# Performance work log

Hardware: AMD Instinct MI355X
Metric: run time of the kernel (lower is better)

## Reference

```python
import jax, jax.numpy as jnp
import numpy as np

USER_COUNT = 100000
ITEM_COUNT = 50000
N_NODES = USER_COUNT + ITEM_COUNT
NNZ = 4800000
EMB = 64
BATCH = 4096


def setup_inputs() -> dict:
    key = jax.random.key(0)
    k1, k2, k3, k4, k5, k6, k7 = jax.random.split(key, 7)
    return {
        "user_emb": jax.random.normal(k1, (USER_COUNT, EMB), dtype=jnp.float32),
        "item_emb": jax.random.normal(k2, (ITEM_COUNT, EMB), dtype=jnp.float32),
        "adj_vals": jax.random.uniform(k3, (NNZ,), dtype=jnp.float32),
        "adj_row": jax.random.randint(k4, (NNZ,), 0, N_NODES, dtype=jnp.int64),
        "adj_col": jax.random.randint(k5, (NNZ,), 0, N_NODES, dtype=jnp.int64),
        "users": jax.random.randint(k6, (BATCH,), 0, USER_COUNT, dtype=jnp.int64),
        "items": jax.random.randint(k7, (BATCH,), 0, ITEM_COUNT, dtype=jnp.int64),
        "n_layers": 3,
    }


def _spmm(adj_row, adj_col, adj_vals, x):
    # sparse (N,N) @ dense (N,D): gather source rows, scale by edge values, scatter-add to dest
    msgs = adj_vals[:, None] * x[adj_col]  # [nnz, D]
    return jax.ops.segment_sum(msgs, adj_row, num_segments=N_NODES)


def reference(user_emb, item_emb, adj_vals, adj_row, adj_col, users, items, n_layers):
    ego = jnp.concatenate([user_emb, item_emb], axis=0)  # [N, D]
    for _ in range(n_layers):
        ego = _spmm(adj_row, adj_col, adj_vals, ego)
    user_all = ego[:USER_COUNT]
    item_all = ego[USER_COUNT:]
    return (user_all[users], item_all[items])
```

## Files before the change

### kernel.cpp

```cpp
#include <hip/hip_runtime.h>
#include <hip/hip_bf16.h>

#define USER_COUNT 100000
#define ITEM_COUNT 50000
#define N_NODES    150000
#define EMB        64
#define BATCH      4096

#define NFINE      586
#define FSHIFT     8
#define STRIDE     8960
#define TILE_E     6400
#define NBSTRIDE   768

__device__ inline unsigned short f2bf_raw(float f) {
    __hip_bfloat16 h = __float2bfloat16(f);
    unsigned short u; __builtin_memcpy(&u, &h, 2); return u;
}

__global__ __launch_bounds__(512) void count_kernel(
        const int* __restrict__ rows, int* __restrict__ counts, int nnz) {
    __shared__ int cnt[NFINE];
    const int b = blockIdx.x, t = threadIdx.x;
    for (int f = t; f < NFINE; f += 512) cnt[f] = 0;
    __syncthreads();
    const int s = b * TILE_E, e = min(s + TILE_E, nnz);
    for (int i = s + t; i < e; i += 512)
        atomicAdd(&cnt[rows[i] >> FSHIFT], 1);
    __syncthreads();
    for (int f = t; f < NFINE; f += 512)
        counts[f * NBSTRIDE + b] = cnt[f];
}

__global__ __launch_bounds__(1024) void scan_offs(
        const int* __restrict__ counts, int* __restrict__ offs,
        int* __restrict__ tot, int nblk) {
    __shared__ int s[1024];
    const int f = blockIdx.x, t = threadIdx.x;
    const int c = (t < nblk) ? counts[f * NBSTRIDE + t] : 0;
    s[t] = c;
    __syncthreads();
    for (int o = 1; o < 1024; o <<= 1) {
        int v = (t >= o) ? s[t - o] : 0;
        __syncthreads();
        s[t] += v;
        __syncthreads();
    }
    if (t < nblk) offs[f * NBSTRIDE + t] = s[t] - c;
    if (t == 1023) tot[f] = s[1023];
}

__global__ __launch_bounds__(512) void partition_kernel(
        const float* __restrict__ vals,
        const int* __restrict__ rows,
        const int* __restrict__ cols,
        const int* __restrict__ offs,
        uint2* __restrict__ fine, int nnz) {
    __shared__ uint2 buf[TILE_E];
    __shared__ int   cnt[NFINE];
    __shared__ int   sloff[NFINE + 1];
    __shared__ int   gb[NFINE];
    __shared__ int   sscan[512];
    const int b = blockIdx.x, t = threadIdx.x;
    const int sbeg = b * TILE_E, send = min(sbeg + TILE_E, nnz);
    const int n = send - sbeg;

    for (int f = t; f < NFINE; f += 512) {
        cnt[f] = 0;
        gb[f] = f * STRIDE + offs[f * NBSTRIDE + b];
    }
    __syncthreads();
    for (int i = sbeg + t; i < send; i += 512)
        atomicAdd(&cnt[rows[i] >> FSHIFT], 1);
    __syncthreads();
    int c0 = (2 * t < NFINE) ? cnt[2 * t] : 0;
    int c1 = (2 * t + 1 < NFINE) ? cnt[2 * t + 1] : 0;
    sscan[t] = c0 + c1;
    __syncthreads();
    for (int o = 1; o < 512; o <<= 1) {
        int v = (t >= o) ? sscan[t - o] : 0;
        __syncthreads();
        sscan[t] += v;
        __syncthreads();
    }
    int base = (t == 0) ? 0 : sscan[t - 1];
    if (2 * t < NFINE) sloff[2 * t] = base;
    if (2 * t + 1 < NFINE) sloff[2 * t + 1] = base + c0;
    if (t == 511) sloff[NFINE] = sscan[511];
    __syncthreads();
    for (int f = t; f < NFINE; f += 512) cnt[f] = sloff[f];
    __syncthreads();
    for (int i = sbeg + t; i < send; i += 512) {
        int r = rows[i];
        int f = r >> FSHIFT;
        int pos = atomicAdd(&cnt[f], 1);
        buf[pos] = make_uint2(__float_as_uint(vals[i]),
                              (unsigned)cols[i] | ((unsigned)(r & 255) << 18));
    }
    __syncthreads();
    for (int idx = t; idx < n; idx += 512) {
        int lo = 0, hi = NFINE;
        while (hi - lo > 1) {
            int mid = (lo + hi) >> 1;
            if (sloff[mid] <= idx) lo = mid; else hi = mid;
        }
        fine[gb[lo] + (idx - sloff[lo])] = buf[idx];
    }
}

__global__ __launch_bounds__(256) void bucket_sort_kernel(
        const uint2* __restrict__ fine,
        const int* __restrict__ tot,
        float2* __restrict__ perm,
        uint2* __restrict__ rp) {
    __shared__ int hist[256];
    __shared__ int off[256];
    __shared__ int cur[256];
    const int f    = blockIdx.x;
    const int tid  = threadIdx.x;
    const int n    = min(tot[f], STRIDE);
    const int base = f * STRIDE;
    const uint2* src = fine + base;

    hist[tid] = 0;
    __syncthreads();
    for (int k = tid; k < n; k += 256)
        atomicAdd(&hist[(src[k].y >> 18) & 255], 1);
    __syncthreads();
    if (tid == 0) {
        int acc = 0;
        for (int j = 0; j < 256; ++j) { off[j] = acc; acc += hist[j]; }
    }
    __syncthreads();
    cur[tid] = off[tid];
    int row = (f << FSHIFT) + tid;
    if (row < N_NODES)
        rp[row] = make_uint2(base + off[tid], base + off[tid] + hist[tid]);
    __syncthreads();
    for (int k = tid; k < n; k += 256) {
        uint2 e = src[k];
        int lrow = (e.y >> 18) & 255;
        int pos = base + atomicAdd(&cur[lrow], 1);
        perm[pos] = make_float2(__uint_as_float(e.x),
                                __int_as_float((int)(e.y & 0x3FFFFu)));
    }
}

__global__ void to_bf16(const float4* __restrict__ ue,
                        const float4* __restrict__ ie,
                        uint2* __restrict__ xh) {
    int i = blockIdx.x * blockDim.x + threadIdx.x;
    const int n4 = (N_NODES * EMB) / 4;
    const int u4 = (USER_COUNT * EMB) / 4;
    if (i >= n4) return;
    float4 fv = (i < u4) ? ue[i] : ie[i - u4];
    uint2 o;
    o.x = (unsigned int)f2bf_raw(fv.x) | ((unsigned int)f2bf_raw(fv.y) << 16);
    o.y = (unsigned int)f2bf_raw(fv.z) | ((unsigned int)f2bf_raw(fv.w) << 16);
    xh[i] = o;
}

#define ACC8(U, W)                                      \
    a0 += (W) * __uint_as_float((U).x << 16);           \
    a1 += (W) * __uint_as_float((U).x & 0xffff0000u);   \
    a2 += (W) * __uint_as_float((U).y << 16);           \
    a3 += (W) * __uint_as_float((U).y & 0xffff0000u);   \
    a4 += (W) * __uint_as_float((U).z << 16);           \
    a5 += (W) * __uint_as_float((U).z & 0xffff0000u);   \
    a6 += (W) * __uint_as_float((U).w << 16);           \
    a7 += (W) * __uint_as_float((U).w & 0xffff0000u);

__global__ void spmm_bf16(const uint2* __restrict__ rp,
                          const float2* __restrict__ perm,
                          const unsigned short* __restrict__ xh,
                          unsigned short* __restrict__ yh) {
    int wid  = (blockIdx.x * blockDim.x + threadIdx.x) >> 6;
    int lane = threadIdx.x & 63;
    int g    = lane >> 3;
    int s    = lane & 7;
    int r    = (wid << 3) + g;
    if (r >= N_NODES) return;

    uint2 be = rp[r];
    int beg = (int)be.x, end = (int)be.y;

    const uint4* xv = (const uint4*)xh;
    float a0 = 0.f, a1 = 0.f, a2 = 0.f, a3 = 0.f;
    float a4 = 0.f, a5 = 0.f, a6 = 0.f, a7 = 0.f;

    int j = beg;
    for (; j + 7 < end; j += 8) {
        float2 e0 = perm[j];
        float2 e1 = perm[j + 1];
        float2 e2 = perm[j + 2];
        float2 e3 = perm[j + 3];
        float2 e4 = perm[j + 4];
        float2 e5 = perm[j + 5];
        float2 e6 = perm[j + 6];
        float2 e7 = perm[j + 7];
        uint4 u0 = xv[(((long long)__float_as_int(e0.y)) << 3) + s];
        uint4 u1 = xv[(((long long)__float_as_int(e1.y)) << 3) + s];
        uint4 u2 = xv[(((long long)__float_as_int(e2.y)) << 3) + s];
        uint4 u3 = xv[(((long long)__float_as_int(e3.y)) << 3) + s];
        uint4 u4 = xv[(((long long)__float_as_int(e4.y)) << 3) + s];
        uint4 u5 = xv[(((long long)__float_as_int(e5.y)) << 3) + s];
        uint4 u6 = xv[(((long long)__float_as_int(e6.y)) << 3) + s];
        uint4 u7 = xv[(((long long)__float_as_int(e7.y)) << 3) + s];
        ACC8(u0, e0.x) ACC8(u1, e1.x) ACC8(u2, e2.x) ACC8(u3, e3.x)
        ACC8(u4, e4.x) ACC8(u5, e5.x) ACC8(u6, e6.x) ACC8(u7, e7.x)
    }
    for (; j < end; ++j) {
        float2 e = perm[j];
        uint4 u = xv[(((long long)__float_as_int(e.y)) << 3) + s];
        ACC8(u, e.x)
    }

    uint4 o;
    o.x = (unsigned)f2bf_raw(a0) | ((unsigned)f2bf_raw(a1) << 16);
    o.y = (unsigned)f2bf_raw(a2) | ((unsigned)f2bf_raw(a3) << 16);
    o.z = (unsigned)f2bf_raw(a4) | ((unsigned)f2bf_raw(a5) << 16);
    o.w = (unsigned)f2bf_raw(a6) | ((unsigned)f2bf_raw(a7) << 16);
    ((uint4*)yh)[(((long long)r) << 3) + s] = o;
}

__global__ void spmm_batch_kernel(const uint2* __restrict__ rp,
                                  const float2* __restrict__ perm,
                                  const unsigned short* __restrict__ xh,
                                  const int* __restrict__ users,
                                  const int* __restrict__ items,
                                  float4* __restrict__ out) {
    int wid  = (blockIdx.x * blockDim.x + threadIdx.x) >> 6;
    int lane = threadIdx.x & 63;
    int g    = lane >> 3;
    int s    = lane & 7;
    int b    = (wid << 3) + g;
    if (b >= 2 * BATCH) return;
    int node = (b < BATCH) ? users[b] : (USER_COUNT + items[b - BATCH]);

    uint2 be = rp[node];
    int beg = (int)be.x, end = (int)be.y;

    const uint4* xv = (const uint4*)xh;
    float a0 = 0.f, a1 = 0.f, a2 = 0.f, a3 = 0.f;
    float a4 = 0.f, a5 = 0.f, a6 = 0.f, a7 = 0.f;

    int j = beg;
    for (; j + 3 < end; j += 4) {
        float2 e0 = perm[j];
        float2 e1 = perm[j + 1];
        float2 e2 = perm[j + 2];
        float2 e3 = perm[j + 3];
        uint4 u0 = xv[(((long long)__float_as_int(e0.y)) << 3) + s];
        uint4 u1 = xv[(((long long)__float_as_int(e1.y)) << 3) + s];
        uint4 u2 = xv[(((long long)__float_as_int(e2.y)) << 3) + s];
        uint4 u3 = xv[(((long long)__float_as_int(e3.y)) << 3) + s];
        ACC8(u0, e0.x) ACC8(u1, e1.x) ACC8(u2, e2.x) ACC8(u3, e3.x)
    }
    for (; j < end; ++j) {
        float2 e = perm[j];
        uint4 u = xv[(((long long)__float_as_int(e.y)) << 3) + s];
        ACC8(u, e.x)
    }

    out[(size_t)b * 16 + 2 * s]     = make_float4(a0, a1, a2, a3);
    out[(size_t)b * 16 + 2 * s + 1] = make_float4(a4, a5, a6, a7);
}

extern "C" void kernel_launch(void* const* d_in, const int* in_sizes, int n_in,
                              void* d_out, int out_size, void* d_ws, size_t ws_size,
                              hipStream_t stream) {
    const float* user_emb = (const float*)d_in[0];
    const float* item_emb = (const float*)d_in[1];
    const float* adj_vals = (const float*)d_in[2];
    const int*   adj_row  = (const int*)d_in[3];
    const int*   adj_col  = (const int*)d_in[4];
    const int*   users    = (const int*)d_in[5];
    const int*   items    = (const int*)d_in[6];

    const int nnz  = in_sizes[2];
    const int nblk = (nnz + TILE_E - 1) / TILE_E;

    const size_t region = (size_t)NFINE * STRIDE + 1024;

    char* p = (char*)d_ws;
    uint2* fine = (uint2*)p;
    unsigned short* xh_a = (unsigned short*)p;
    unsigned short* xh_b = xh_a + (size_t)N_NODES * EMB;
    p += region * sizeof(uint2);
    float2* perm = (float2*)p;
    p += region * sizeof(float2);
    uint2* rp = (uint2*)p;
    p += (size_t)(N_NODES + 16) * sizeof(uint2);
    int* counts = (int*)p;  p += (size_t)NFINE * NBSTRIDE * sizeof(int);
    int* offs   = (int*)p;  p += (size_t)NFINE * NBSTRIDE * sizeof(int);
    int* tot    = (int*)p;

    count_kernel<<<nblk, 512, 0, stream>>>(adj_row, counts, nnz);
    scan_offs<<<NFINE, 1024, 0, stream>>>(counts, offs, tot, nblk);
    partition_kernel<<<nblk, 512, 0, stream>>>(adj_vals, adj_row, adj_col,
                                               offs, fine, nnz);
    bucket_sort_kernel<<<NFINE, 256, 0, stream>>>(fine, tot, perm, rp);

    const int n4 = (N_NODES * EMB) / 4;
    to_bf16<<<(n4 + 255) / 256, 256, 0, stream>>>((const float4*)user_emb,
                                                  (const float4*)item_emb,
                                                  (uint2*)xh_a);

    const int spmm_blocks = (N_NODES / 8 + 3) / 4;
    spmm_bf16<<<spmm_blocks, 256, 0, stream>>>(rp, perm, xh_a, xh_b);
    spmm_bf16<<<spmm_blocks, 256, 0, stream>>>(rp, perm, xh_b, xh_a);
    spmm_batch_kernel<<<(2 * BATCH / 8) / 4, 256, 0, stream>>>(
        rp, perm, xh_a, users, items, (float4*)d_out);
}
```

Baseline: 440.6 us.

## Replace two-level bucket sort with global-atomic counting sort for CSR build

```diff
diff --git a/kernel.cpp b/kernel.cpp
--- a/kernel.cpp
+++ b/kernel.cpp
@@ -7,142 +7,114 @@
 #define EMB        64
 #define BATCH      4096
 
-#define NFINE      586
-#define FSHIFT     8
-#define STRIDE     8960
-#define TILE_E     6400
-#define NBSTRIDE   768
+#define SCAN_BLOCKS 147
 
 __device__ inline unsigned short f2bf_raw(float f) {
     __hip_bfloat16 h = __float2bfloat16(f);
     unsigned short u; __builtin_memcpy(&u, &h, 2); return u;
 }
 
-__global__ __launch_bounds__(512) void count_kernel(
-        const int* __restrict__ rows, int* __restrict__ counts, int nnz) {
-    __shared__ int cnt[NFINE];
-    const int b = blockIdx.x, t = threadIdx.x;
-    for (int f = t; f < NFINE; f += 512) cnt[f] = 0;
+__global__ __launch_bounds__(256) void zero_kernel(int* __restrict__ p, int n) {
+    int i = blockIdx.x * blockDim.x + threadIdx.x;
+    if (i < n) p[i] = 0;
+}
+
+__global__ __launch_bounds__(256) void degree_kernel(
+        const int* __restrict__ rows, int* __restrict__ deg, int nnz) {
+    const int tid = blockIdx.x * blockDim.x + threadIdx.x;
+    const int nth = gridDim.x * blockDim.x;
+    const int n4  = nnz >> 2;
+    const int4* r4 = (const int4*)rows;
+    for (int i = tid; i < n4; i += nth) {
+        int4 r = r4[i];
+        atomicAdd(&deg[r.x], 1);
+        atomicAdd(&deg[r.y], 1);
+        atomicAdd(&deg[r.z], 1);
+        atomicAdd(&deg[r.w], 1);
+    }
+    for (int i = (n4 << 2) + tid; i < nnz; i += nth)
+        atomicAdd(&deg[rows[i]], 1);
+}
+
+__global__ __launch_bounds__(1024) void scan_reduce(
+        const int* __restrict__ deg, int* __restrict__ bsum) {
+    __shared__ int s[1024];
+    const int t = threadIdx.x;
+    const int idx = blockIdx.x * 1024 + t;
+    s[t] = (idx < N_NODES) ? deg[idx] : 0;
     __syncthreads();
-    const int s = b * TILE_E, e = min(s + TILE_E, nnz);
-    for (int i = s + t; i < e; i += 512)
-        atomicAdd(&cnt[rows[i] >> FSHIFT], 1);
+    for (int o = 512; o > 0; o >>= 1) {
+        if (t < o) s[t] += s[t + o];
+        __syncthreads();
+    }
+    if (t == 0) bsum[blockIdx.x] = s[0];
+}
+
+__global__ __launch_bounds__(256) void scan_mid(int* __restrict__ bsum, int nb) {
+    __shared__ int s[256];
+    const int t = threadIdx.x;
+    const int v = (t < nb) ? bsum[t] : 0;
+    s[t] = v;
     __syncthreads();
-    for (int f = t; f < NFINE; f += 512)
-        counts[f * NBSTRIDE + b] = cnt[f];
-}
-
-__global__ __launch_bounds__(1024) void scan_offs(
-        const int* __restrict__ counts, int* __restrict__ offs,
-        int* __restrict__ tot, int nblk) {
+    for (int o = 1; o < 256; o <<= 1) {
+        int x = (t >= o) ? s[t - o] : 0;
+        __syncthreads();
+        s[t] += x;
+        __syncthreads();
+    }
+    if (t < nb) bsum[t] = s[t] - v;
+}
+
+__global__ __launch_bounds__(1024) void scan_final(
+        const int* __restrict__ deg, const int* __restrict__ bsum,
+        uint2* __restrict__ rp, int* __restrict__ cursor) {
     __shared__ int s[1024];
-    const int f = blockIdx.x, t = threadIdx.x;
-    const int c = (t < nblk) ? counts[f * NBSTRIDE + t] : 0;
-    s[t] = c;
+    const int t = threadIdx.x;
+    const int idx = blockIdx.x * 1024 + t;
+    const int v = (idx < N_NODES) ? deg[idx] : 0;
+    s[t] = v;
     __syncthreads();
     for (int o = 1; o < 1024; o <<= 1) {
-        int v = (t >= o) ? s[t - o] : 0;
-        __syncthreads();
-        s[t] += v;
-        __syncthreads();
-    }
-    if (t < nblk) offs[f * NBSTRIDE + t] = s[t] - c;
-    if (t == 1023) tot[f] = s[1023];
-}
-
-__global__ __launch_bounds__(512) void partition_kernel(
+        int x = (t >= o) ? s[t - o] : 0;
+        __syncthreads();
+        s[t] += x;
+        __syncthreads();
+    }
+    if (idx < N_NODES) {
+        int excl = s[t] - v + bsum[blockIdx.x];
+        rp[idx]     = make_uint2((unsigned)excl, (unsigned)(excl + v));
+        cursor[idx] = excl;
+    }
+}
+
+__global__ __launch_bounds__(256) void scatter_kernel(
         const float* __restrict__ vals,
         const int* __restrict__ rows,
         const int* __restrict__ cols,
-        const int* __restrict__ offs,
-        uint2* __restrict__ fine, int nnz) {
-    __shared__ uint2 buf[TILE_E];
-    __shared__ int   cnt[NFINE];
-    __shared__ int   sloff[NFINE + 1];
-    __shared__ int   gb[NFINE];
-    __shared__ int   sscan[512];
-    const int b = blockIdx.x, t = threadIdx.x;
-    const int sbeg = b * TILE_E, send = min(sbeg + TILE_E, nnz);
-    const int n = send - sbeg;
-
-    for (int f = t; f < NFINE; f += 512) {
-        cnt[f] = 0;
-        gb[f] = f * STRIDE + offs[f * NBSTRIDE + b];
-    }
-    __syncthreads();
-    for (int i = sbeg + t; i < send; i += 512)
-        atomicAdd(&cnt[rows[i] >> FSHIFT], 1);
-    __syncthreads();
-    int c0 = (2 * t < NFINE) ? cnt[2 * t] : 0;
-    int c1 = (2 * t + 1 < NFINE) ? cnt[2 * t + 1] : 0;
-    sscan[t] = c0 + c1;
-    __syncthreads();
-    for (int o = 1; o < 512; o <<= 1) {
-        int v = (t >= o) ? sscan[t - o] : 0;
-        __syncthreads();
-        sscan[t] += v;
-        __syncthreads();
-    }
-    int base = (t == 0) ? 0 : sscan[t - 1];
-    if (2 * t < NFINE) sloff[2 * t] = base;
-    if (2 * t + 1 < NFINE) sloff[2 * t + 1] = base + c0;
-    if (t == 511) sloff[NFINE] = sscan[511];
-    __syncthreads();
-    for (int f = t; f < NFINE; f += 512) cnt[f] = sloff[f];
-    __syncthreads();
-    for (int i = sbeg + t; i < send; i += 512) {
-        int r = rows[i];
-        int f = r >> FSHIFT;
-        int pos = atomicAdd(&cnt[f], 1);
-        buf[pos] = make_uint2(__float_as_uint(vals[i]),
-                              (unsigned)cols[i] | ((unsigned)(r & 255) << 18));
-    }
-    __syncthreads();
-    for (int idx = t; idx < n; idx += 512) {
-        int lo = 0, hi = NFINE;
-        while (hi - lo > 1) {
-            int mid = (lo + hi) >> 1;
-            if (sloff[mid] <= idx) lo = mid; else hi = mid;
-        }
-        fine[gb[lo] + (idx - sloff[lo])] = buf[idx];
-    }
-}
-
-__global__ __launch_bounds__(256) void bucket_sort_kernel(
-        const uint2* __restrict__ fine,
-        const int* __restrict__ tot,
-        float2* __restrict__ perm,
-        uint2* __restrict__ rp) {
-    __shared__ int hist[256];
-    __shared__ int off[256];
-    __shared__ int cur[256];
-    const int f    = blockIdx.x;
-    const int tid  = threadIdx.x;
-    const int n    = min(tot[f], STRIDE);
-    const int base = f * STRIDE;
-    const uint2* src = fine + base;
-
-    hist[tid] = 0;
-    __syncthreads();
-    for (int k = tid; k < n; k += 256)
-        atomicAdd(&hist[(src[k].y >> 18) & 255], 1);
-    __syncthreads();
-    if (tid == 0) {
-        int acc = 0;
-        for (int j = 0; j < 256; ++j) { off[j] = acc; acc += hist[j]; }
-    }
-    __syncthreads();
-    cur[tid] = off[tid];
-    int row = (f << FSHIFT) + tid;
-    if (row < N_NODES)
-        rp[row] = make_uint2(base + off[tid], base + off[tid] + hist[tid]);
-    __syncthreads();
-    for (int k = tid; k < n; k += 256) {
-        uint2 e = src[k];
-        int lrow = (e.y >> 18) & 255;
-        int pos = base + atomicAdd(&cur[lrow], 1);
-        perm[pos] = make_float2(__uint_as_float(e.x),
-                                __int_as_float((int)(e.y & 0x3FFFFu)));
+        int* __restrict__ cursor,
+        float2* __restrict__ perm, int nnz) {
+    const int tid = blockIdx.x * blockDim.x + threadIdx.x;
+    const int nth = gridDim.x * blockDim.x;
+    const int n4  = nnz >> 2;
+    const int4*   r4 = (const int4*)rows;
+    const int4*   c4 = (const int4*)cols;
+    const float4* v4 = (const float4*)vals;
+    for (int i = tid; i < n4; i += nth) {
+        int4   r = r4[i];
+        int4   c = c4[i];
+        float4 v = v4[i];
+        int p0 = atomicAdd(&cursor[r.x], 1);
+        int p1 = atomicAdd(&cursor[r.y], 1);
+        int p2 = atomicAdd(&cursor[r.z], 1);
+        int p3 = atomicAdd(&cursor[r.w], 1);
+        perm[p0] = make_float2(v.x, __int_as_float(c.x));
+        perm[p1] = make_float2(v.y, __int_as_float(c.y));
+        perm[p2] = make_float2(v.z, __int_as_float(c.z));
+        perm[p3] = make_float2(v.w, __int_as_float(c.w));
+    }
+    for (int i = (n4 << 2) + tid; i < nnz; i += nth) {
+        int p = atomicAdd(&cursor[rows[i]], 1);
+        perm[p] = make_float2(vals[i], __int_as_float(cols[i]));
     }
 }
 
@@ -277,29 +249,31 @@
     const int*   users    = (const int*)d_in[5];
     const int*   items    = (const int*)d_in[6];
 
-    const int nnz  = in_sizes[2];
-    const int nblk = (nnz + TILE_E - 1) / TILE_E;
-
-    const size_t region = (size_t)NFINE * STRIDE + 1024;
+    const int nnz = in_sizes[2];
 
     char* p = (char*)d_ws;
-    uint2* fine = (uint2*)p;
+    float2* perm = (float2*)p;
+    p += (size_t)nnz * sizeof(float2);
     unsigned short* xh_a = (unsigned short*)p;
-    unsigned short* xh_b = xh_a + (size_t)N_NODES * EMB;
-    p += region * sizeof(uint2);
-    float2* perm = (float2*)p;
-    p += region * sizeof(float2);
+    p += (size_t)N_NODES * EMB * sizeof(unsigned short);
+    unsigned short* xh_b = (unsigned short*)p;
+    p += (size_t)N_NODES * EMB * sizeof(unsigned short);
     uint2* rp = (uint2*)p;
     p += (size_t)(N_NODES + 16) * sizeof(uint2);
-    int* counts = (int*)p;  p += (size_t)NFINE * NBSTRIDE * sizeof(int);
-    int* offs   = (int*)p;  p += (size_t)NFINE * NBSTRIDE * sizeof(int);
-    int* tot    = (int*)p;
-
-    count_kernel<<<nblk, 512, 0, stream>>>(adj_row, counts, nnz);
-    scan_offs<<<NFINE, 1024, 0, stream>>>(counts, offs, tot, nblk);
-    partition_kernel<<<nblk, 512, 0, stream>>>(adj_vals, adj_row, adj_col,
-                                               offs, fine, nnz);
-    bucket_sort_kernel<<<NFINE, 256, 0, stream>>>(fine, tot, perm, rp);
+    int* deg = (int*)p;
+    p += (size_t)(N_NODES + 64) * sizeof(int);
+    int* cursor = (int*)p;
+    p += (size_t)(N_NODES + 64) * sizeof(int);
+    int* bsum = (int*)p;
+    p += 1024 * sizeof(int);
+
+    zero_kernel<<<(N_NODES + 255) / 256, 256, 0, stream>>>(deg, N_NODES);
+    degree_kernel<<<2048, 256, 0, stream>>>(adj_row, deg, nnz);
+    scan_reduce<<<SCAN_BLOCKS, 1024, 0, stream>>>(deg, bsum);
+    scan_mid<<<1, 256, 0, stream>>>(bsum, SCAN_BLOCKS);
+    scan_final<<<SCAN_BLOCKS, 1024, 0, stream>>>(deg, bsum, rp, cursor);
+    scatter_kernel<<<2048, 256, 0, stream>>>(adj_vals, adj_row, adj_col,
+                                             cursor, perm, nnz);
 
     const int n4 = (N_NODES * EMB) / 4;
     to_bf16<<<(n4 + 255) / 256, 256, 0, stream>>>((const float4*)user_emb,
```

Measured after the change: 866.8 us. 1.97x slower.

## Replace count+scan pre-pass with global atomic bucket reservation in partition

Applied to the files above, without the earlier changes.

```diff
diff --git a/kernel.cpp b/kernel.cpp
--- a/kernel.cpp
+++ b/kernel.cpp
@@ -11,52 +11,25 @@
 #define FSHIFT     8
 #define STRIDE     8960
 #define TILE_E     6400
-#define NBSTRIDE   768
 
 __device__ inline unsigned short f2bf_raw(float f) {
     __hip_bfloat16 h = __float2bfloat16(f);
     unsigned short u; __builtin_memcpy(&u, &h, 2); return u;
 }
 
-__global__ __launch_bounds__(512) void count_kernel(
-        const int* __restrict__ rows, int* __restrict__ counts, int nnz) {
-    __shared__ int cnt[NFINE];
-    const int b = blockIdx.x, t = threadIdx.x;
-    for (int f = t; f < NFINE; f += 512) cnt[f] = 0;
-    __syncthreads();
-    const int s = b * TILE_E, e = min(s + TILE_E, nnz);
-    for (int i = s + t; i < e; i += 512)
-        atomicAdd(&cnt[rows[i] >> FSHIFT], 1);
-    __syncthreads();
-    for (int f = t; f < NFINE; f += 512)
-        counts[f * NBSTRIDE + b] = cnt[f];
-}
-
-__global__ __launch_bounds__(1024) void scan_offs(
-        const int* __restrict__ counts, int* __restrict__ offs,
-        int* __restrict__ tot, int nblk) {
-    __shared__ int s[1024];
-    const int f = blockIdx.x, t = threadIdx.x;
-    const int c = (t < nblk) ? counts[f * NBSTRIDE + t] : 0;
-    s[t] = c;
-    __syncthreads();
-    for (int o = 1; o < 1024; o <<= 1) {
-        int v = (t >= o) ? s[t - o] : 0;
-        __syncthreads();
-        s[t] += v;
-        __syncthreads();
-    }
-    if (t < nblk) offs[f * NBSTRIDE + t] = s[t] - c;
-    if (t == 1023) tot[f] = s[1023];
+__global__ __launch_bounds__(256) void zero_kernel(int* __restrict__ p, int n) {
+    int i = blockIdx.x * blockDim.x + threadIdx.x;
+    if (i < n) p[i] = 0;
 }
 
 __global__ __launch_bounds__(512) void partition_kernel(
         const float* __restrict__ vals,
         const int* __restrict__ rows,
         const int* __restrict__ cols,
-        const int* __restrict__ offs,
+        int* __restrict__ gcur,
         uint2* __restrict__ fine, int nnz) {
     __shared__ uint2 buf[TILE_E];
+    __shared__ unsigned short bid[TILE_E];
     __shared__ int   cnt[NFINE];
     __shared__ int   sloff[NFINE + 1];
     __shared__ int   gb[NFINE];
@@ -65,10 +38,7 @@
     const int sbeg = b * TILE_E, send = min(sbeg + TILE_E, nnz);
     const int n = send - sbeg;
 
-    for (int f = t; f < NFINE; f += 512) {
-        cnt[f] = 0;
-        gb[f] = f * STRIDE + offs[f * NBSTRIDE + b];
-    }
+    for (int f = t; f < NFINE; f += 512) cnt[f] = 0;
     __syncthreads();
     for (int i = sbeg + t; i < send; i += 512)
         atomicAdd(&cnt[rows[i] >> FSHIFT], 1);
@@ -88,7 +58,11 @@
     if (2 * t + 1 < NFINE) sloff[2 * t + 1] = base + c0;
     if (t == 511) sloff[NFINE] = sscan[511];
     __syncthreads();
-    for (int f = t; f < NFINE; f += 512) cnt[f] = sloff[f];
+    for (int f = t; f < NFINE; f += 512) {
+        int c = cnt[f];
+        gb[f] = f * STRIDE + ((c > 0) ? atomicAdd(&gcur[f], c) : 0);
+        cnt[f] = sloff[f];
+    }
     __syncthreads();
     for (int i = sbeg + t; i < send; i += 512) {
         int r = rows[i];
@@ -96,49 +70,55 @@
         int pos = atomicAdd(&cnt[f], 1);
         buf[pos] = make_uint2(__float_as_uint(vals[i]),
                               (unsigned)cols[i] | ((unsigned)(r & 255) << 18));
+        bid[pos] = (unsigned short)f;
     }
     __syncthreads();
     for (int idx = t; idx < n; idx += 512) {
-        int lo = 0, hi = NFINE;
-        while (hi - lo > 1) {
-            int mid = (lo + hi) >> 1;
-            if (sloff[mid] <= idx) lo = mid; else hi = mid;
-        }
-        fine[gb[lo] + (idx - sloff[lo])] = buf[idx];
-    }
-}
-
-__global__ __launch_bounds__(256) void bucket_sort_kernel(
+        int f = bid[idx];
+        fine[gb[f] + (idx - sloff[f])] = buf[idx];
+    }
+}
+
+__global__ __launch_bounds__(512) void bucket_sort_kernel(
         const uint2* __restrict__ fine,
         const int* __restrict__ tot,
         float2* __restrict__ perm,
         uint2* __restrict__ rp) {
+    __shared__ uint2 sbuf[STRIDE];
     __shared__ int hist[256];
-    __shared__ int off[256];
     __shared__ int cur[256];
-    const int f    = blockIdx.x;
-    const int tid  = threadIdx.x;
-    const int n    = min(tot[f], STRIDE);
+    __shared__ int ss[256];
+    const int f   = blockIdx.x;
+    const int t   = threadIdx.x;
+    const int n   = min(tot[f], STRIDE);
     const int base = f * STRIDE;
-    const uint2* src = fine + base;
-
-    hist[tid] = 0;
-    __syncthreads();
-    for (int k = tid; k < n; k += 256)
-        atomicAdd(&hist[(src[k].y >> 18) & 255], 1);
-    __syncthreads();
-    if (tid == 0) {
-        int acc = 0;
-        for (int j = 0; j < 256; ++j) { off[j] = acc; acc += hist[j]; }
-    }
-    __syncthreads();
-    cur[tid] = off[tid];
-    int row = (f << FSHIFT) + tid;
-    if (row < N_NODES)
-        rp[row] = make_uint2(base + off[tid], base + off[tid] + hist[tid]);
-    __syncthreads();
-    for (int k = tid; k < n; k += 256) {
-        uint2 e = src[k];
+
+    if (t < 256) hist[t] = 0;
+    for (int k = t; k < n; k += 512) sbuf[k] = fine[base + k];
+    __syncthreads();
+    for (int k = t; k < n; k += 512)
+        atomicAdd(&hist[(sbuf[k].y >> 18) & 255], 1);
+    __syncthreads();
+    int v = (t < 256) ? hist[t] : 0;
+    if (t < 256) ss[t] = v;
+    __syncthreads();
+    for (int o = 1; o < 256; o <<= 1) {
+        int x = (t < 256 && t >= o) ? ss[t - o] : 0;
+        __syncthreads();
+        if (t < 256) ss[t] += x;
+        __syncthreads();
+    }
+    if (t < 256) {
+        int e = ss[t] - v;
+        cur[t] = e;
+        int row = (f << FSHIFT) + t;
+        if (row < N_NODES)
+            rp[row] = make_uint2((unsigned)(base + e),
+                                 (unsigned)(base + e + v));
+    }
+    __syncthreads();
+    for (int k = t; k < n; k += 512) {
+        uint2 e = sbuf[k];
         int lrow = (e.y >> 18) & 255;
         int pos = base + atomicAdd(&cur[lrow], 1);
         perm[pos] = make_float2(__uint_as_float(e.x),
@@ -291,15 +271,13 @@
     p += region * sizeof(float2);
     uint2* rp = (uint2*)p;
     p += (size_t)(N_NODES + 16) * sizeof(uint2);
-    int* counts = (int*)p;  p += (size_t)NFINE * NBSTRIDE * sizeof(int);
-    int* offs   = (int*)p;  p += (size_t)NFINE * NBSTRIDE * sizeof(int);
-    int* tot    = (int*)p;
-
-    count_kernel<<<nblk, 512, 0, stream>>>(adj_row, counts, nnz);
-    scan_offs<<<NFINE, 1024, 0, stream>>>(counts, offs, tot, nblk);
+    int* gcur = (int*)p;
+    p += 1024 * sizeof(int);
+
+    zero_kernel<<<4, 256, 0, stream>>>(gcur, 1024);
     partition_kernel<<<nblk, 512, 0, stream>>>(adj_vals, adj_row, adj_col,
-                                               offs, fine, nnz);
-    bucket_sort_kernel<<<NFINE, 256, 0, stream>>>(fine, tot, perm, rp);
+                                               gcur, fine, nnz);
+    bucket_sort_kernel<<<NFINE, 512, 0, stream>>>(fine, gcur, perm, rp);
 
     const int n4 = (N_NODES * EMB) / 4;
     to_bf16<<<(n4 + 255) / 256, 256, 0, stream>>>((const float4*)user_emb,
```

Result: faster. 419.2 us (-4.9%).
